# Kernel optimization log

Hardware: AMD Instinct MI355X
Metric: run time of the kernel (lower is better)

## Reference

```python
import jax, jax.numpy as jnp
import numpy as np

T_STEPS, BATCH, DX, DH = 128, 128, 1024, 1024
N_GATES = 5


def setup_inputs() -> dict:
    key = jax.random.key(0)
    ks = jax.random.split(key, 4)
    scale_x = 1.0 / np.sqrt(DX)
    scale_h = 1.0 / np.sqrt(DH)
    inputs = jax.random.normal(ks[0], (T_STEPS, BATCH, DX), dtype=jnp.float32)
    memories = jax.random.normal(ks[1], (T_STEPS, BATCH, DH), dtype=jnp.float32)
    h0 = jnp.zeros((BATCH, DH), dtype=jnp.float32)
    c0 = jnp.zeros((BATCH, DH), dtype=jnp.float32)
    Wx = jax.random.normal(ks[2], (N_GATES * DH, DX), dtype=jnp.float32) * scale_x
    bx = jnp.zeros((N_GATES * DH,), dtype=jnp.float32)
    Wh = jax.random.normal(ks[3], (N_GATES * DH, DH), dtype=jnp.float32) * scale_h
    # forget-gate bias (second chunk) initialized to 1, as in reset_parameters_
    bh = jnp.zeros((N_GATES * DH,), dtype=jnp.float32).at[DH:2 * DH].set(1.0)
    return {"inputs": inputs, "memories": memories, "h0": h0, "c0": c0,
            "Wx": Wx, "bx": bx, "Wh": Wh, "bh": bh}


def reference(inputs, memories, h0, c0, Wx, bx, Wh, bh):
    # EpLSTMCell.loop: time-major scan of the custom gated cell.
    # Gate order: I, F, G, O, R (tied forget gate: it = 1 - ft).
    def step(carry, inp):
        h, c = carry
        xt, mt = inp
        gx = jnp.dot(xt, Wx.T) + bx      # [B, 5*Dh]
        gh = jnp.dot(h, Wh.T) + bh       # [B, 5*Dh]
        Xi, Xf, Xg, Xo, Xr = jnp.split(gx, N_GATES, axis=-1)
        Hi, Hf, Hg, Ho, Hr = jnp.split(gh, N_GATES, axis=-1)
        ft = jax.nn.sigmoid(Xf + Hf)
        ot = jax.nn.sigmoid(Xo + Ho)
        it = 1.0 - ft                    # tied forget gate
        gt = jnp.tanh(Xg + Hg)
        rt = jax.nn.sigmoid(Xr + Hr)     # episodic memory gate
        ct = ft * c + it * gt + rt * jnp.tanh(mt)
        ht = ot * jnp.tanh(ct)
        return (ht, ct), ht

    (_, _), outs = jax.lax.scan(step, (h0, c0), (inputs, memories))
    return outs  # [T, B, Dh]
```

## Files before the change

kernel.cpp:

```cpp
#include <hip/hip_runtime.h>

#define T_STEPS 128
#define BATCH   128
#define DX      1024
#define DH      1024
#define BDH     (BATCH * DH)
#define BDX     (BATCH * DX)
#define PLW     40

typedef __attribute__((ext_vector_type(8)))  short short8;
typedef __attribute__((ext_vector_type(16))) float f32x16;

static __device__ __forceinline__ unsigned short f2bf(float f) {
    union { float f; unsigned u; } v; v.f = f;
    unsigned r = v.u + 0x7fffu + ((v.u >> 16) & 1u);
    return (unsigned short)(r >> 16);
}
static __device__ __forceinline__ float sigf(float x) {
    float u = __expf(-fabsf(x));
    float b = 1.0f / (1.0f + u);
    return x >= 0.0f ? b : 1.0f - b;
}
static __device__ __forceinline__ float tanhfast(float x) {
    float u = __expf(-2.0f * fabsf(x));
    float r = (1.0f - u) / (1.0f + u);
    return x >= 0.0f ? r : -r;
}


__global__ __launch_bounds__(256) void prep_x(const float* __restrict__ x,
                                              unsigned short* __restrict__ Xb) {
    const size_t i8 = ((size_t)blockIdx.x * 256 + threadIdx.x) * 8;
    float4 lo = reinterpret_cast<const float4*>(x + i8)[0];
    float4 hi = reinterpret_cast<const float4*>(x + i8)[1];
    union { unsigned short u[8]; short8 v; } pk;
    pk.u[0]=f2bf(lo.x); pk.u[1]=f2bf(lo.y); pk.u[2]=f2bf(lo.z); pk.u[3]=f2bf(lo.w);
    pk.u[4]=f2bf(hi.x); pk.u[5]=f2bf(hi.y); pk.u[6]=f2bf(hi.z); pk.u[7]=f2bf(hi.w);
    *reinterpret_cast<short8*>(Xb + i8) = pk.v;
}

__global__ __launch_bounds__(256) void init_seed(const float* __restrict__ h0,
                                                 unsigned short* __restrict__ hseq,
                                                 unsigned* __restrict__ gflag) {
    const int i = blockIdx.x * 256 + threadIdx.x;
    if (i < BDH) hseq[i] = f2bf(h0[i]);
    if (blockIdx.x == 0) gflag[threadIdx.x] = 0;
}

__global__ __launch_bounds__(128) void prep_wxp(const float* __restrict__ Wx,
                                                const float* __restrict__ bx,
                                                const float* __restrict__ bh,
                                                unsigned short* __restrict__ Wxp,
                                                float* __restrict__ bp) {
    const int p = blockIdx.x;
    const int js = p >> 5, g = (p >> 3) & 3, jj = p & 7;
    const int srow = (g + 1) * 1024 + js * 8 + jj;
    const int k = threadIdx.x * 8;
    float4 lo = *(const float4*)(Wx + (size_t)srow * DX + k);
    float4 hi = *(const float4*)(Wx + (size_t)srow * DX + k + 4);
    union { unsigned short u[8]; short8 v; } pk;
    pk.u[0]=f2bf(lo.x); pk.u[1]=f2bf(lo.y); pk.u[2]=f2bf(lo.z); pk.u[3]=f2bf(lo.w);
    pk.u[4]=f2bf(hi.x); pk.u[5]=f2bf(hi.y); pk.u[6]=f2bf(hi.z); pk.u[7]=f2bf(hi.w);
    *reinterpret_cast<short8*>(Wxp + (size_t)p * 1024 + k) = pk.v;
    if (threadIdx.x == 0) bp[p] = bx[srow] + bh[srow];
}

template<bool XBF16>
__global__ __launch_bounds__(256, 1) void gx_prepass2(
    const void* __restrict__ xsrc, const unsigned short* __restrict__ Wxp,
    const float* __restrict__ bp, _Float16* __restrict__ Gx)
{
    extern __shared__ char sm[];
    _Float16* pl16 = (_Float16*)(sm + 131072);

    const int bid = blockIdx.x;
    const int c  = bid & 7;
    const int jp = bid >> 3;
    const int tid = threadIdx.x;

    {
        const int row = tid >> 2;
        const int chunk = tid & 3;
        const int sw = (row & 7) << 4;
        const unsigned short* src = Wxp + (size_t)(jp * 64 + row) * 1024;
        char* dst = sm + row * 2048;
        #pragma unroll
        for (int j = 0; j < 32; ++j) {
            const int off = chunk * 16 + j * 64;
            short8 v = *(const short8*)(src + (off >> 1));
            *(short8*)(dst + (off ^ sw)) = v;
        }
    }

    const int rrow = tid >> 1;
    const int jjb  = (tid & 1) * 4;
    float bias_f[2][16];
    #pragma unroll
    for (int jsl = 0; jsl < 2; ++jsl)
        #pragma unroll
        for (int q = 0; q < 4; ++q)
            #pragma unroll
            for (int g = 0; g < 4; ++g)
                bias_f[jsl][q * 4 + g] = bp[(jp * 2 + jsl) * 32 + g * 8 + (jjb + q)];

    const int wave = tid >> 6, lane = tid & 63;
    const int k8 = (lane >> 5) * 8;
    const char* wrow0 = sm + (lane & 31) * 2048;
    const char* wrow1 = wrow0 + 32 * 2048;
    const int sw2 = ((lane & 31) & 7) << 4;
    __syncthreads();

    for (int i = 0; i < 16; ++i) {
        const int mt = c * 16 + i;
        const int arow = mt * 128 + wave * 32 + (lane & 31);
        f32x16 a00 = {}, a01 = {}, a10 = {}, a11 = {};

        if (XBF16) {
            const unsigned short* xp = (const unsigned short*)xsrc + (size_t)arow * 1024 + k8;
            #pragma unroll 8
            for (int ks = 0; ks < 64; ++ks) {
                short8 a  = *(const short8*)(xp + ks * 16);
                short8 b0 = *(const short8*)(wrow0 + ((ks * 32 + k8 * 2) ^ sw2));
                short8 b1 = *(const short8*)(wrow1 + ((ks * 32 + k8 * 2) ^ sw2));
                if (ks & 1) {
                    a01 = __builtin_amdgcn_mfma_f32_32x32x16_bf16(a, b0, a01, 0, 0, 0);
                    a11 = __builtin_amdgcn_mfma_f32_32x32x16_bf16(a, b1, a11, 0, 0, 0);
                } else {
                    a00 = __builtin_amdgcn_mfma_f32_32x32x16_bf16(a, b0, a00, 0, 0, 0);
                    a10 = __builtin_amdgcn_mfma_f32_32x32x16_bf16(a, b1, a10, 0, 0, 0);
                }
            }
        } else {
            const float* Af = (const float*)xsrc + (size_t)arow * 1024 + k8;
            #pragma unroll 8
            for (int ks = 0; ks < 64; ++ks) {
                float4 lo = *(const float4*)(Af + ks * 16);
                float4 hi = *(const float4*)(Af + ks * 16 + 4);
                union { unsigned u32[4]; short8 v; } pk;
                pk.u32[0] = __builtin_amdgcn_perm(__float_as_uint(lo.y), __float_as_uint(lo.x), 0x07060302u);
                pk.u32[1] = __builtin_amdgcn_perm(__float_as_uint(lo.w), __float_as_uint(lo.z), 0x07060302u);
                pk.u32[2] = __builtin_amdgcn_perm(__float_as_uint(hi.y), __float_as_uint(hi.x), 0x07060302u);
                pk.u32[3] = __builtin_amdgcn_perm(__float_as_uint(hi.w), __float_as_uint(hi.z), 0x07060302u);
                short8 b0 = *(const short8*)(wrow0 + ((ks * 32 + k8 * 2) ^ sw2));
                short8 b1 = *(const short8*)(wrow1 + ((ks * 32 + k8 * 2) ^ sw2));
                if (ks & 1) {
                    a01 = __builtin_amdgcn_mfma_f32_32x32x16_bf16(pk.v, b0, a01, 0, 0, 0);
                    a11 = __builtin_amdgcn_mfma_f32_32x32x16_bf16(pk.v, b1, a11, 0, 0, 0);
                } else {
                    a00 = __builtin_amdgcn_mfma_f32_32x32x16_bf16(pk.v, b0, a00, 0, 0, 0);
                    a10 = __builtin_amdgcn_mfma_f32_32x32x16_bf16(pk.v, b1, a10, 0, 0, 0);
                }
            }
        }
        f32x16 r0 = a00 + a01;
        f32x16 r1 = a10 + a11;

        #pragma unroll
        for (int ii = 0; ii < 16; ++ii) {
            const int rowc = (ii & 3) + 8 * (ii >> 2) + 4 * (lane >> 5);
            pl16[(wave * 32 + rowc) * 72 + (lane & 31)]      = (_Float16)r0[ii];
            pl16[(wave * 32 + rowc) * 72 + 32 + (lane & 31)] = (_Float16)r1[ii];
        }
        __syncthreads();

        #pragma unroll
        for (int jsl = 0; jsl < 2; ++jsl) {
            __attribute__((aligned(16))) _Float16 vals[16];
            #pragma unroll
            for (int q = 0; q < 4; ++q)
                #pragma unroll
                for (int g = 0; g < 4; ++g)
                    vals[q * 4 + g] = (_Float16)(
                        (float)pl16[rrow * 72 + jsl * 32 + g * 8 + (jjb + q)]
                        + bias_f[jsl][q * 4 + g]);
            _Float16* dst = Gx + ((size_t)(mt * 128 + rrow) * 4096
                                  + (jp * 2 + jsl) * 32 + jjb * 4);
            *(uint4*)dst       = *(uint4*)&vals[0];
            *(uint4*)(dst + 8) = *(uint4*)&vals[8];
        }
        __syncthreads();
    }
}

__global__ __launch_bounds__(256, 1) void eplstm_h(
    const _Float16* __restrict__ Gx,  const float* __restrict__ mem,
    const float* __restrict__ Wh,     const float* __restrict__ c0,
    unsigned short* __restrict__ hseq, float* __restrict__ out,
    unsigned* __restrict__ gflag)
{
    extern __shared__ char smem[];
    float* pl = (float*)(smem + 65536);

    const int bid = blockIdx.x;
    const int js = bid >> 1, bhh = bid & 1;
    const int tid = threadIdx.x;

    {
        const int row = tid >> 3;
        const int g = row >> 3, jj = row & 7;
        const int srow = (g + 1) * 1024 + js * 8 + jj;
        const int sw = (row & 7) << 4;
        const float* W = Wh + (size_t)srow * 1024;
        char* dst = smem + row * 2048;
        #pragma unroll
        for (int it = 0; it < 16; ++it) {
            const int k = (tid & 7) * 128 + it * 8;
            float4 lo = *(const float4*)(W + k);
            float4 hi = *(const float4*)(W + k + 4);
            union { unsigned short u[8]; short8 v; } pk;
            pk.u[0]=f2bf(lo.x); pk.u[1]=f2bf(lo.y); pk.u[2]=f2bf(lo.z); pk.u[3]=f2bf(lo.w);
            pk.u[4]=f2bf(hi.x); pk.u[5]=f2bf(hi.y); pk.u[6]=f2bf(hi.z); pk.u[7]=f2bf(hi.w);
            *(short8*)(dst + ((k * 2) ^ sw)) = pk.v;
        }
    }

    const int e0 = tid * 2;
    const int row_e = e0 >> 3;
    const int jj0 = e0 & 7;
    const int brow = bhh * 64 + row_e;
    const size_t obase = (size_t)brow * DH + js * 8 + jj0;
    const int mh_e = row_e >> 5, r_e = row_e & 31;
    float2 creg = *(const float2*)(c0 + obase);

    const int wave = tid >> 6, lane = tid & 63;
    const int mh = wave >> 1, kh = wave & 1;
    const int arow = bhh * 64 + mh * 32 + (lane & 31);
    const int k8 = (lane >> 5) * 8;
    const char* wrow = smem + (lane & 31) * 2048;
    const int sw2 = ((lane & 31) & 7) << 4;
    const int kbyte0 = (kh * 512 + k8) * 2;
    const int p = lane & 31;
    const int word = (p & 7) * 4 + (p >> 3);
    float* plw = pl + wave * 32 * PLW;
    unsigned long long* fb = (unsigned long long*)(gflag + bhh * 128);

    __syncthreads();

    for (int t = 0; t < T_STEPS; ++t) {
        uint4 gxv = *(const uint4*)(Gx + ((size_t)(t * BATCH + brow) * 4096 + js * 32 + jj0 * 4));
        float2 mv = *(const float2*)(mem + (size_t)t * BDH + obase);

        if (t > 0) {
            for (;;) {
                unsigned long long fv = __hip_atomic_load(&fb[lane], __ATOMIC_RELAXED,
                                                          __HIP_MEMORY_SCOPE_AGENT);
                if (__all(((unsigned)fv >= (unsigned)t) &&
                          ((unsigned)(fv >> 32) >= (unsigned)t))) break;
                __builtin_amdgcn_s_sleep(1);
            }
        }

        const unsigned short* hp = hseq + (size_t)t * BDH + (size_t)arow * DH + kh * 512 + k8;
        f32x16 a0 = {}, a1 = {};
        #pragma unroll 16
        for (int ks = 0; ks < 32; ++ks) {
            short8 a = *(const short8*)(hp + ks * 16);
            short8 b = *(const short8*)(wrow + ((kbyte0 + ks * 32) ^ sw2));
            if (ks & 1) a1 = __builtin_amdgcn_mfma_f32_32x32x16_bf16(a, b, a1, 0, 0, 0);
            else        a0 = __builtin_amdgcn_mfma_f32_32x32x16_bf16(a, b, a0, 0, 0, 0);
        }
        f32x16 r = a0 + a1;
        #pragma unroll
        for (int ii = 0; ii < 16; ++ii) {
            const int rowc = (ii & 3) + 8 * (ii >> 2) + 4 * (lane >> 5);
            plw[rowc * PLW + word] = r[ii];
        }
        __syncthreads();

        float4 p0A = *(const float4*)(pl + (((mh_e << 1) | 0) * 32 + r_e) * PLW + (jj0 + 0) * 4);
        float4 p0B = *(const float4*)(pl + (((mh_e << 1) | 1) * 32 + r_e) * PLW + (jj0 + 0) * 4);
        float4 p1A = *(const float4*)(pl + (((mh_e << 1) | 0) * 32 + r_e) * PLW + (jj0 + 1) * 4);
        float4 p1B = *(const float4*)(pl + (((mh_e << 1) | 1) * 32 + r_e) * PLW + (jj0 + 1) * 4);
        union { uint4 u; _Float16 h[8]; } G; G.u = gxv;

        float hv[2];
        {
            const float gF = (float)G.h[0] + p0A.x + p0B.x;
            const float gG = (float)G.h[1] + p0A.y + p0B.y;
            const float gO = (float)G.h[2] + p0A.z + p0B.z;
            const float gR = (float)G.h[3] + p0A.w + p0B.w;
            const float ft = sigf(gF), ot = sigf(gO), rt = sigf(gR);
            const float gt = tanhfast(gG);
            const float cv = ft * creg.x + (1.f - ft) * gt + rt * tanhfast(mv.x);
            creg.x = cv;
            hv[0] = ot * tanhfast(cv);
        }
        {
            const float gF = (float)G.h[4] + p1A.x + p1B.x;
            const float gG = (float)G.h[5] + p1A.y + p1B.y;
            const float gO = (float)G.h[6] + p1A.z + p1B.z;
            const float gR = (float)G.h[7] + p1A.w + p1B.w;
            const float ft = sigf(gF), ot = sigf(gO), rt = sigf(gR);
            const float gt = tanhfast(gG);
            const float cv = ft * creg.y + (1.f - ft) * gt + rt * tanhfast(mv.y);
            creg.y = cv;
            hv[1] = ot * tanhfast(cv);
        }
        *(float2*)(out + (size_t)t * BDH + obase) = make_float2(hv[0], hv[1]);
        const unsigned hp2 = (unsigned)f2bf(hv[0]) | ((unsigned)f2bf(hv[1]) << 16);
        __hip_atomic_store((unsigned*)(hseq + (size_t)(t + 1) * BDH + obase), hp2,
                           __ATOMIC_RELAXED, __HIP_MEMORY_SCOPE_AGENT);

        asm volatile("s_waitcnt vmcnt(0)" ::: "memory");
        __syncthreads();
        if (tid == 0 && t < T_STEPS - 1) {
            __hip_atomic_store(&gflag[bhh * 128 + js], (unsigned)(t + 1),
                               __ATOMIC_RELAXED, __HIP_MEMORY_SCOPE_AGENT);
        }
    }
}

template<bool XBF16>
__global__ __launch_bounds__(256, 1) void eplstm_persistent(
    const void*  __restrict__ xsrc, const float* __restrict__ mem,
    const float* __restrict__ Wx,   const float* __restrict__ Wh,
    const float* __restrict__ bxp,  const float* __restrict__ bhp,
    const float* __restrict__ c0,
    unsigned short* __restrict__ hseq, float* __restrict__ out,
    unsigned* __restrict__ bar)
{
    extern __shared__ char smem[];
    float* pl = reinterpret_cast<float*>(smem + 131072);

    const int bid = blockIdx.x;
    const int js  = bid >> 1;
    const int bhh = bid & 1;
    const int tid = threadIdx.x;

    {
        const int prow = tid >> 3;
        const int g = prow >> 3, jj = prow & 7;
        const int srow = (g + 1) * 1024 + js * 8 + jj;
        const int kc = (tid & 7) * 256;
        const int sw = (prow & 7) << 4;
        for (int it = 0; it < 32; ++it) {
            const int k = kc + it * 8;
            const float* src = (k < DX) ? (Wx + (size_t)srow * DX + k)
                                        : (Wh + (size_t)srow * DH + (k - DX));
            float4 lo = reinterpret_cast<const float4*>(src)[0];
            float4 hi = reinterpret_cast<const float4*>(src)[1];
            union { unsigned short u[8]; short8 v; } pk;
            pk.u[0]=f2bf(lo.x); pk.u[1]=f2bf(lo.y); pk.u[2]=f2bf(lo.z); pk.u[3]=f2bf(lo.w);
            pk.u[4]=f2bf(hi.x); pk.u[5]=f2bf(hi.y); pk.u[6]=f2bf(hi.z); pk.u[7]=f2bf(hi.w);
            *reinterpret_cast<short8*>(smem + prow * 4096 + ((k * 2) ^ sw)) = pk.v;
        }
    }

    const int e0   = tid * 2;
    const int bl   = e0 >> 3;
    const int jj0  = e0 & 7;
    const int brow_g = bhh * 64 + bl;
    const size_t oidx = (size_t)brow_g * DH + js * 8 + jj0;
    float biasv[2][4];
    #pragma unroll
    for (int e2 = 0; e2 < 2; ++e2)
        #pragma unroll
        for (int g = 0; g < 4; ++g) {
            const int srow = (g + 1) * 1024 + js * 8 + jj0 + e2;
            biasv[e2][g] = bxp[srow] + bhp[srow];
        }
    float2 creg = *reinterpret_cast<const float2*>(c0 + oidx);
    const int mh_e = bl >> 5, rr = bl & 31;

    const int wave = tid >> 6;
    const int lane = tid & 63;
    const int mh = wave >> 1, kh = wave & 1;
    const int arow   = bhh * 64 + mh * 32 + (lane & 31);
    const int k8     = (lane >> 5) * 8;
    const int brow   = lane & 31;
    const char* bbase = smem + brow * 4096;
    const int swz    = (brow & 7) << 4;
    const int kbyte0 = kh * 2048 + k8 * 2;

    __syncthreads();

    for (int t = 0; t < T_STEPS; ++t) {
        f32x16 ac0 = {}, ac1 = {}, ac2 = {}, ac3 = {};
        if (XBF16 || kh == 1) {
            const unsigned short* Ab = kh
                ? (hseq + (size_t)t * BDH + (size_t)arow * DH + k8)
                : ((const unsigned short*)xsrc + (size_t)t * BDX + (size_t)arow * DX + k8);
            #pragma unroll 8
            for (int ks = 0; ks < 64; ++ks) {
                short8 a = *reinterpret_cast<const short8*>(Ab + ks * 16);
                short8 b = *reinterpret_cast<const short8*>(bbase + ((kbyte0 + ks * 32) ^ swz));
                if      ((ks & 3) == 0) ac0 = __builtin_amdgcn_mfma_f32_32x32x16_bf16(a, b, ac0, 0, 0, 0);
                else if ((ks & 3) == 1) ac1 = __builtin_amdgcn_mfma_f32_32x32x16_bf16(a, b, ac1, 0, 0, 0);
                else if ((ks & 3) == 2) ac2 = __builtin_amdgcn_mfma_f32_32x32x16_bf16(a, b, ac2, 0, 0, 0);
                else                    ac3 = __builtin_amdgcn_mfma_f32_32x32x16_bf16(a, b, ac3, 0, 0, 0);
            }
        } else {
            const float* Af = (const float*)xsrc + (size_t)t * BDX + (size_t)arow * DX + k8;
            #pragma unroll 4
            for (int ks = 0; ks < 64; ++ks) {
                float4 lo = reinterpret_cast<const float4*>(Af + ks * 16)[0];
                float4 hi = reinterpret_cast<const float4*>(Af + ks * 16)[1];
                union { unsigned short u[8]; short8 v; } pk;
                pk.u[0]=f2bf(lo.x); pk.u[1]=f2bf(lo.y); pk.u[2]=f2bf(lo.z); pk.u[3]=f2bf(lo.w);
                pk.u[4]=f2bf(hi.x); pk.u[5]=f2bf(hi.y); pk.u[6]=f2bf(hi.z); pk.u[7]=f2bf(hi.w);
                short8 a = pk.v;
                short8 b = *reinterpret_cast<const short8*>(bbase + ((kbyte0 + ks * 32) ^ swz));
                if      ((ks & 3) == 0) ac0 = __builtin_amdgcn_mfma_f32_32x32x16_bf16(a, b, ac0, 0, 0, 0);
                else if ((ks & 3) == 1) ac1 = __builtin_amdgcn_mfma_f32_32x32x16_bf16(a, b, ac1, 0, 0, 0);
                else if ((ks & 3) == 2) ac2 = __builtin_amdgcn_mfma_f32_32x32x16_bf16(a, b, ac2, 0, 0, 0);
                else                    ac3 = __builtin_amdgcn_mfma_f32_32x32x16_bf16(a, b, ac3, 0, 0, 0);
            }
        }
        f32x16 r = (ac0 + ac1) + (ac2 + ac3);

        #pragma unroll
        for (int i = 0; i < 16; ++i) {
            const int row = (i & 3) + 8 * (i >> 2) + 4 * (lane >> 5);
            pl[(wave * 32 + row) * 33 + brow] = r[i];
        }
        __syncthreads();

        const float2 mt2 = *reinterpret_cast<const float2*>(mem + (size_t)t * BDH + oidx);
        float hv[2];
        #pragma unroll
        for (int e2 = 0; e2 < 2; ++e2) {
            const int jj = jj0 + e2;
            float gs[4];
            #pragma unroll
            for (int g = 0; g < 4; ++g) {
                const int col = g * 8 + jj;
                gs[g] = pl[((mh_e * 2 + 0) * 32 + rr) * 33 + col]
                      + pl[((mh_e * 2 + 1) * 32 + rr) * 33 + col]
                      + biasv[e2][g];
            }
            const float ft = 1.f / (1.f + expf(-gs[0]));
            const float gt = tanhf(gs[1]);
            const float ot = 1.f / (1.f + expf(-gs[2]));
            const float rt = 1.f / (1.f + expf(-gs[3]));
            const float cin = e2 ? creg.y : creg.x;
            const float mv  = e2 ? mt2.y : mt2.x;
            const float cv = ft * cin + (1.f - ft) * gt + rt * tanhf(mv);
            if (e2) creg.y = cv; else creg.x = cv;
            hv[e2] = ot * tanhf(cv);
        }
        *reinterpret_cast<float2*>(out + (size_t)t * BDH + oidx) = make_float2(hv[0], hv[1]);
        const unsigned hp = (unsigned)f2bf(hv[0]) | ((unsigned)f2bf(hv[1]) << 16);
        __hip_atomic_store((unsigned*)(hseq + (size_t)(t + 1) * BDH + oidx), hp,
                           __ATOMIC_RELAXED, __HIP_MEMORY_SCOPE_AGENT);

        __syncthreads();
        if (t < T_STEPS - 1) {
            if (tid == 0) {
                const unsigned want = (unsigned)(t + 1);
                const unsigned arrived = __hip_atomic_fetch_add(
                    &bar[bhh * 32], 1u, __ATOMIC_RELAXED, __HIP_MEMORY_SCOPE_AGENT);
                if (arrived == want * 128u - 1u) {
                    __hip_atomic_store(&bar[64 + bhh * 32], want,
                                       __ATOMIC_RELAXED, __HIP_MEMORY_SCOPE_AGENT);
                } else {
                    while (__hip_atomic_load(&bar[64 + bhh * 32],
                                             __ATOMIC_RELAXED, __HIP_MEMORY_SCOPE_AGENT) < want)
                        __builtin_amdgcn_s_sleep(2);
                }
            }
            __syncthreads();
        }
    }
}

extern "C" void kernel_launch(void* const* d_in, const int* in_sizes, int n_in,
                              void* d_out, int out_size, void* d_ws, size_t ws_size,
                              hipStream_t stream) {
    const float* inputs   = (const float*)d_in[0];
    const float* memories = (const float*)d_in[1];
    const float* h0       = (const float*)d_in[2];
    const float* c0       = (const float*)d_in[3];
    const float* Wx       = (const float*)d_in[4];
    const float* bx       = (const float*)d_in[5];
    const float* Wh       = (const float*)d_in[6];
    const float* bh_      = (const float*)d_in[7];
    float* outp = (float*)d_out;

    char* ws = (char*)d_ws;
    size_t off = 0;
    auto alloc = [&](size_t bytes) {
        char* p = ws + off;
        off = (off + bytes + 255) & ~(size_t)255;
        return p;
    };
    unsigned*       gflag = (unsigned*)alloc(256 * sizeof(unsigned));
    unsigned short* hseq  = (unsigned short*)alloc((size_t)(T_STEPS + 1) * BDH * 2);

    const size_t wxp_b  = (size_t)4096 * 1024 * 2;
    const size_t bp_b   = 4096 * 4;
    const size_t gx_b   = (size_t)16384 * 4096 * 2;
    const size_t xb_b   = (size_t)T_STEPS * BDX * 2;
    const size_t need_base = off + wxp_b + 256 + bp_b + 256 + gx_b + 256;
    const size_t need_xb   = need_base + xb_b + 256;

    if (ws_size >= need_base) {
        unsigned short* Wxp = (unsigned short*)alloc(wxp_b);
        float*          bp  = (float*)alloc(bp_b);
        _Float16*       Gx  = (_Float16*)alloc(gx_b);
        const bool use_xb = (ws_size >= need_xb);
        unsigned short* Xb = use_xb ? (unsigned short*)alloc(xb_b) : nullptr;

        init_seed<<<512, 256, 0, stream>>>(h0, hseq, gflag);
        prep_wxp<<<4096, 128, 0, stream>>>(Wx, bx, bh_, Wxp, bp);

        const unsigned pre_smem = 131072 + 128 * 72 * 2;
        if (use_xb) {
            prep_x<<<8192, 256, 0, stream>>>(inputs, Xb);
            (void)hipFuncSetAttribute((const void*)gx_prepass2<true>,
                                      hipFuncAttributeMaxDynamicSharedMemorySize, pre_smem);
            gx_prepass2<true><<<512, 256, pre_smem, stream>>>((const void*)Xb, Wxp, bp, Gx);
        } else {
            (void)hipFuncSetAttribute((const void*)gx_prepass2<false>,
                                      hipFuncAttributeMaxDynamicSharedMemorySize, pre_smem);
            gx_prepass2<false><<<512, 256, pre_smem, stream>>>((const void*)inputs, Wxp, bp, Gx);
        }

        const unsigned smem_bytes = 65536 + 4 * 32 * PLW * 4;
        (void)hipFuncSetAttribute((const void*)eplstm_h,
                                  hipFuncAttributeMaxDynamicSharedMemorySize, smem_bytes);
        void* kargs[] = { (void*)&Gx, (void*)&memories, (void*)&Wh, (void*)&c0,
                          (void*)&hseq, (void*)&outp, (void*)&gflag };
        hipError_t err = hipLaunchCooperativeKernel((const void*)eplstm_h, dim3(256),
                                                    dim3(256), kargs, smem_bytes, stream);
        if (err != hipSuccess) {
            eplstm_h<<<256, 256, smem_bytes, stream>>>(Gx, memories, Wh, c0,
                                                       hseq, outp, gflag);
        }
    } else {
        const bool use_xb = (ws_size >= off + xb_b + 256);
        unsigned short* Xb = use_xb ? (unsigned short*)alloc(xb_b) : nullptr;

        init_seed<<<512, 256, 0, stream>>>(h0, hseq, gflag);
        if (use_xb) prep_x<<<8192, 256, 0, stream>>>(inputs, Xb);

        const unsigned smem_bytes = 131072 + 9216 + 9216 + 64;
        const void* xsrc = use_xb ? (const void*)Xb : (const void*)inputs;
        if (use_xb) {
            (void)hipFuncSetAttribute((const void*)eplstm_persistent<true>,
                                      hipFuncAttributeMaxDynamicSharedMemorySize, smem_bytes);
            void* kargs[] = { (void*)&xsrc, (void*)&memories, (void*)&Wx, (void*)&Wh,
                              (void*)&bx, (void*)&bh_, (void*)&c0, (void*)&hseq,
                              (void*)&outp, (void*)&gflag };
            hipError_t err = hipLaunchCooperativeKernel(
                (const void*)eplstm_persistent<true>, dim3(256), dim3(256),
                kargs, smem_bytes, stream);
            if (err != hipSuccess) {
                eplstm_persistent<true><<<256, 256, smem_bytes, stream>>>(
                    xsrc, memories, Wx, Wh, bx, bh_, c0, hseq, outp, gflag);
            }
        } else {
            (void)hipFuncSetAttribute((const void*)eplstm_persistent<false>,
                                      hipFuncAttributeMaxDynamicSharedMemorySize, smem_bytes);
            void* kargs[] = { (void*)&xsrc, (void*)&memories, (void*)&Wx, (void*)&Wh,
                              (void*)&bx, (void*)&bh_, (void*)&c0, (void*)&hseq,
                              (void*)&outp, (void*)&gflag };
            hipError_t err = hipLaunchCooperativeKernel(
                (const void*)eplstm_persistent<false>, dim3(256), dim3(256),
                kargs, smem_bytes, stream);
            if (err != hipSuccess) {
                eplstm_persistent<false><<<256, 256, smem_bytes, stream>>>(
                    xsrc, memories, Wx, Wh, bx, bh_, c0, hseq, outp, gflag);
            }
        }
    }
}
```

Measured before the change: 1.554 ms.

## Use nontemporal loads/stores and single-wave flag polling in recurrent kernel

Replaces many streaming global loads and stores (weight conversion, Gx writes/reads, memory and output tensors) with nontemporal variants so they bypass or deprioritise the cache. In the recurrent loop, only wave 0 now polls the cross-block step flags, with a longer sleep, and the other waves wait at a block barrier. The output store moves after the hseq publish. The flag buffer is also doubled and zero-initialised. The intent is to cut cache pollution and polling traffic, at the cost of an extra barrier per step and possibly slower wake-up.

```diff
diff --git a/kernel.cpp b/kernel.cpp
--- a/kernel.cpp
+++ b/kernel.cpp
@@ -10,12 +10,21 @@
 
 typedef __attribute__((ext_vector_type(8)))  short short8;
 typedef __attribute__((ext_vector_type(16))) float f32x16;
+typedef __attribute__((ext_vector_type(4)))  float f32x4v;
+typedef __attribute__((ext_vector_type(2)))  float f32x2;
+typedef __attribute__((ext_vector_type(4)))  unsigned u32x4;
 
 static __device__ __forceinline__ unsigned short f2bf(float f) {
     union { float f; unsigned u; } v; v.f = f;
     unsigned r = v.u + 0x7fffu + ((v.u >> 16) & 1u);
     return (unsigned short)(r >> 16);
 }
+static __device__ __forceinline__ short8 pack_bf16x8(f32x4v lo, f32x4v hi) {
+    union { unsigned short u[8]; short8 v; } pk;
+    pk.u[0]=f2bf(lo[0]); pk.u[1]=f2bf(lo[1]); pk.u[2]=f2bf(lo[2]); pk.u[3]=f2bf(lo[3]);
+    pk.u[4]=f2bf(hi[0]); pk.u[5]=f2bf(hi[1]); pk.u[6]=f2bf(hi[2]); pk.u[7]=f2bf(hi[3]);
+    return pk.v;
+}
 static __device__ __forceinline__ float sigf(float x) {
     float u = __expf(-fabsf(x));
     float b = 1.0f / (1.0f + u);
@@ -31,12 +40,10 @@
 __global__ __launch_bounds__(256) void prep_x(const float* __restrict__ x,
                                               unsigned short* __restrict__ Xb) {
     const size_t i8 = ((size_t)blockIdx.x * 256 + threadIdx.x) * 8;
-    float4 lo = reinterpret_cast<const float4*>(x + i8)[0];
-    float4 hi = reinterpret_cast<const float4*>(x + i8)[1];
-    union { unsigned short u[8]; short8 v; } pk;
-    pk.u[0]=f2bf(lo.x); pk.u[1]=f2bf(lo.y); pk.u[2]=f2bf(lo.z); pk.u[3]=f2bf(lo.w);
-    pk.u[4]=f2bf(hi.x); pk.u[5]=f2bf(hi.y); pk.u[6]=f2bf(hi.z); pk.u[7]=f2bf(hi.w);
-    *reinterpret_cast<short8*>(Xb + i8) = pk.v;
+    f32x4v lo = __builtin_nontemporal_load((const f32x4v*)(x + i8));
+    f32x4v hi = __builtin_nontemporal_load((const f32x4v*)(x + i8 + 4));
+    short8 v = pack_bf16x8(lo, hi);
+    __builtin_nontemporal_store(v, (short8*)(Xb + i8));
 }
 
 __global__ __launch_bounds__(256) void init_seed(const float* __restrict__ h0,
@@ -44,7 +51,7 @@
                                                  unsigned* __restrict__ gflag) {
     const int i = blockIdx.x * 256 + threadIdx.x;
     if (i < BDH) hseq[i] = f2bf(h0[i]);
-    if (blockIdx.x == 0) gflag[threadIdx.x] = 0;
+    if (blockIdx.x < 2) gflag[blockIdx.x * 256 + threadIdx.x] = 0;
 }
 
 __global__ __launch_bounds__(128) void prep_wxp(const float* __restrict__ Wx,
@@ -56,12 +63,10 @@
     const int js = p >> 5, g = (p >> 3) & 3, jj = p & 7;
     const int srow = (g + 1) * 1024 + js * 8 + jj;
     const int k = threadIdx.x * 8;
-    float4 lo = *(const float4*)(Wx + (size_t)srow * DX + k);
-    float4 hi = *(const float4*)(Wx + (size_t)srow * DX + k + 4);
-    union { unsigned short u[8]; short8 v; } pk;
-    pk.u[0]=f2bf(lo.x); pk.u[1]=f2bf(lo.y); pk.u[2]=f2bf(lo.z); pk.u[3]=f2bf(lo.w);
-    pk.u[4]=f2bf(hi.x); pk.u[5]=f2bf(hi.y); pk.u[6]=f2bf(hi.z); pk.u[7]=f2bf(hi.w);
-    *reinterpret_cast<short8*>(Wxp + (size_t)p * 1024 + k) = pk.v;
+    f32x4v lo = __builtin_nontemporal_load((const f32x4v*)(Wx + (size_t)srow * DX + k));
+    f32x4v hi = __builtin_nontemporal_load((const f32x4v*)(Wx + (size_t)srow * DX + k + 4));
+    short8 v = pack_bf16x8(lo, hi);
+    __builtin_nontemporal_store(v, (short8*)(Wxp + (size_t)p * 1024 + k));
     if (threadIdx.x == 0) bp[p] = bx[srow] + bh[srow];
 }
 
@@ -87,7 +92,7 @@
         #pragma unroll
         for (int j = 0; j < 32; ++j) {
             const int off = chunk * 16 + j * 64;
-            short8 v = *(const short8*)(src + (off >> 1));
+            short8 v = __builtin_nontemporal_load((const short8*)(src + (off >> 1)));
             *(short8*)(dst + (off ^ sw)) = v;
         }
     }
@@ -134,13 +139,13 @@
             const float* Af = (const float*)xsrc + (size_t)arow * 1024 + k8;
             #pragma unroll 8
             for (int ks = 0; ks < 64; ++ks) {
-                float4 lo = *(const float4*)(Af + ks * 16);
-                float4 hi = *(const float4*)(Af + ks * 16 + 4);
+                f32x4v lo = *(const f32x4v*)(Af + ks * 16);
+                f32x4v hi = *(const f32x4v*)(Af + ks * 16 + 4);
                 union { unsigned u32[4]; short8 v; } pk;
-                pk.u32[0] = __builtin_amdgcn_perm(__float_as_uint(lo.y), __float_as_uint(lo.x), 0x07060302u);
-                pk.u32[1] = __builtin_amdgcn_perm(__float_as_uint(lo.w), __float_as_uint(lo.z), 0x07060302u);
-                pk.u32[2] = __builtin_amdgcn_perm(__float_as_uint(hi.y), __float_as_uint(hi.x), 0x07060302u);
-                pk.u32[3] = __builtin_amdgcn_perm(__float_as_uint(hi.w), __float_as_uint(hi.z), 0x07060302u);
+                pk.u32[0] = __builtin_amdgcn_perm(__float_as_uint(lo[1]), __float_as_uint(lo[0]), 0x07060302u);
+                pk.u32[1] = __builtin_amdgcn_perm(__float_as_uint(lo[3]), __float_as_uint(lo[2]), 0x07060302u);
+                pk.u32[2] = __builtin_amdgcn_perm(__float_as_uint(hi[1]), __float_as_uint(hi[0]), 0x07060302u);
+                pk.u32[3] = __builtin_amdgcn_perm(__float_as_uint(hi[3]), __float_as_uint(hi[2]), 0x07060302u);
                 short8 b0 = *(const short8*)(wrow0 + ((ks * 32 + k8 * 2) ^ sw2));
                 short8 b1 = *(const short8*)(wrow1 + ((ks * 32 + k8 * 2) ^ sw2));
                 if (ks & 1) {
@@ -165,18 +170,18 @@
 
         #pragma unroll
         for (int jsl = 0; jsl < 2; ++jsl) {
-            __attribute__((aligned(16))) _Float16 vals[16];
+            union { _Float16 h[16]; u32x4 q[2]; } V;
             #pragma unroll
             for (int q = 0; q < 4; ++q)
                 #pragma unroll
                 for (int g = 0; g < 4; ++g)
-                    vals[q * 4 + g] = (_Float16)(
+                    V.h[q * 4 + g] = (_Float16)(
                         (float)pl16[rrow * 72 + jsl * 32 + g * 8 + (jjb + q)]
                         + bias_f[jsl][q * 4 + g]);
             _Float16* dst = Gx + ((size_t)(mt * 128 + rrow) * 4096
                                   + (jp * 2 + jsl) * 32 + jjb * 4);
-            *(uint4*)dst       = *(uint4*)&vals[0];
-            *(uint4*)(dst + 8) = *(uint4*)&vals[8];
+            __builtin_nontemporal_store(V.q[0], (u32x4*)dst);
+            __builtin_nontemporal_store(V.q[1], (u32x4*)(dst + 8));
         }
         __syncthreads();
     }
@@ -205,12 +210,10 @@
         #pragma unroll
         for (int it = 0; it < 16; ++it) {
             const int k = (tid & 7) * 128 + it * 8;
-            float4 lo = *(const float4*)(W + k);
-            float4 hi = *(const float4*)(W + k + 4);
-            union { unsigned short u[8]; short8 v; } pk;
-            pk.u[0]=f2bf(lo.x); pk.u[1]=f2bf(lo.y); pk.u[2]=f2bf(lo.z); pk.u[3]=f2bf(lo.w);
-            pk.u[4]=f2bf(hi.x); pk.u[5]=f2bf(hi.y); pk.u[6]=f2bf(hi.z); pk.u[7]=f2bf(hi.w);
-            *(short8*)(dst + ((k * 2) ^ sw)) = pk.v;
+            f32x4v lo = __builtin_nontemporal_load((const f32x4v*)(W + k));
+            f32x4v hi = __builtin_nontemporal_load((const f32x4v*)(W + k + 4));
+            short8 v = pack_bf16x8(lo, hi);
+            *(short8*)(dst + ((k * 2) ^ sw)) = v;
         }
     }
 
@@ -237,17 +240,22 @@
     __syncthreads();
 
     for (int t = 0; t < T_STEPS; ++t) {
-        uint4 gxv = *(const uint4*)(Gx + ((size_t)(t * BATCH + brow) * 4096 + js * 32 + jj0 * 4));
-        float2 mv = *(const float2*)(mem + (size_t)t * BDH + obase);
+        u32x4 gxv = __builtin_nontemporal_load(
+            (const u32x4*)(Gx + ((size_t)(t * BATCH + brow) * 4096 + js * 32 + jj0 * 4)));
+        f32x2 mv = __builtin_nontemporal_load(
+            (const f32x2*)(mem + (size_t)t * BDH + obase));
 
         if (t > 0) {
-            for (;;) {
-                unsigned long long fv = __hip_atomic_load(&fb[lane], __ATOMIC_RELAXED,
-                                                          __HIP_MEMORY_SCOPE_AGENT);
-                if (__all(((unsigned)fv >= (unsigned)t) &&
-                          ((unsigned)(fv >> 32) >= (unsigned)t))) break;
-                __builtin_amdgcn_s_sleep(1);
-            }
+            if (wave == 0) {
+                for (;;) {
+                    unsigned long long fv = __hip_atomic_load(
+                        &fb[lane], __ATOMIC_RELAXED, __HIP_MEMORY_SCOPE_AGENT);
+                    if (__all(((unsigned)fv >= (unsigned)t) &&
+                              ((unsigned)(fv >> 32) >= (unsigned)t))) break;
+                    __builtin_amdgcn_s_sleep(4);
+                }
+            }
+            __syncthreads();
         }
 
         const unsigned short* hp = hseq + (size_t)t * BDH + (size_t)arow * DH + kh * 512 + k8;
@@ -271,7 +279,7 @@
         float4 p0B = *(const float4*)(pl + (((mh_e << 1) | 1) * 32 + r_e) * PLW + (jj0 + 0) * 4);
         float4 p1A = *(const float4*)(pl + (((mh_e << 1) | 0) * 32 + r_e) * PLW + (jj0 + 1) * 4);
         float4 p1B = *(const float4*)(pl + (((mh_e << 1) | 1) * 32 + r_e) * PLW + (jj0 + 1) * 4);
-        union { uint4 u; _Float16 h[8]; } G; G.u = gxv;
+        union { u32x4 u; _Float16 h[8]; } G; G.u = gxv;
 
         float hv[2];
         {
@@ -281,7 +289,7 @@
             const float gR = (float)G.h[3] + p0A.w + p0B.w;
             const float ft = sigf(gF), ot = sigf(gO), rt = sigf(gR);
             const float gt = tanhfast(gG);
-            const float cv = ft * creg.x + (1.f - ft) * gt + rt * tanhfast(mv.x);
+            const float cv = ft * creg.x + (1.f - ft) * gt + rt * tanhfast(mv[0]);
             creg.x = cv;
             hv[0] = ot * tanhfast(cv);
         }
@@ -292,14 +300,15 @@
             const float gR = (float)G.h[7] + p1A.w + p1B.w;
             const float ft = sigf(gF), ot = sigf(gO), rt = sigf(gR);
             const float gt = tanhfast(gG);
-            const float cv = ft * creg.y + (1.f - ft) * gt + rt * tanhfast(mv.y);
+            const float cv = ft * creg.y + (1.f - ft) * gt + rt * tanhfast(mv[1]);
             creg.y = cv;
             hv[1] = ot * tanhfast(cv);
         }
-        *(float2*)(out + (size_t)t * BDH + obase) = make_float2(hv[0], hv[1]);
         const unsigned hp2 = (unsigned)f2bf(hv[0]) | ((unsigned)f2bf(hv[1]) << 16);
         __hip_atomic_store((unsigned*)(hseq + (size_t)(t + 1) * BDH + obase), hp2,
                            __ATOMIC_RELAXED, __HIP_MEMORY_SCOPE_AGENT);
+        f32x2 hvv = { hv[0], hv[1] };
+        __builtin_nontemporal_store(hvv, (f32x2*)(out + (size_t)t * BDH + obase));
 
         asm volatile("s_waitcnt vmcnt(0)" ::: "memory");
         __syncthreads();
@@ -337,12 +346,10 @@
             const int k = kc + it * 8;
             const float* src = (k < DX) ? (Wx + (size_t)srow * DX + k)
                                         : (Wh + (size_t)srow * DH + (k - DX));
-            float4 lo = reinterpret_cast<const float4*>(src)[0];
-            float4 hi = reinterpret_cast<const float4*>(src)[1];
-            union { unsigned short u[8]; short8 v; } pk;
-            pk.u[0]=f2bf(lo.x); pk.u[1]=f2bf(lo.y); pk.u[2]=f2bf(lo.z); pk.u[3]=f2bf(lo.w);
-            pk.u[4]=f2bf(hi.x); pk.u[5]=f2bf(hi.y); pk.u[6]=f2bf(hi.z); pk.u[7]=f2bf(hi.w);
-            *reinterpret_cast<short8*>(smem + prow * 4096 + ((k * 2) ^ sw)) = pk.v;
+            f32x4v lo = *(const f32x4v*)(src);
+            f32x4v hi = *(const f32x4v*)(src + 4);
+            short8 v = pack_bf16x8(lo, hi);
+            *reinterpret_cast<short8*>(smem + prow * 4096 + ((k * 2) ^ sw)) = v;
         }
     }
 
@@ -393,12 +400,9 @@
             const float* Af = (const float*)xsrc + (size_t)t * BDX + (size_t)arow * DX + k8;
             #pragma unroll 4
             for (int ks = 0; ks < 64; ++ks) {
-                float4 lo = reinterpret_cast<const float4*>(Af + ks * 16)[0];
-                float4 hi = reinterpret_cast<const float4*>(Af + ks * 16)[1];
-                union { unsigned short u[8]; short8 v; } pk;
-                pk.u[0]=f2bf(lo.x); pk.u[1]=f2bf(lo.y); pk.u[2]=f2bf(lo.z); pk.u[3]=f2bf(lo.w);
-                pk.u[4]=f2bf(hi.x); pk.u[5]=f2bf(hi.y); pk.u[6]=f2bf(hi.z); pk.u[7]=f2bf(hi.w);
-                short8 a = pk.v;
+                f32x4v lo = *(const f32x4v*)(Af + ks * 16);
+                f32x4v hi = *(const f32x4v*)(Af + ks * 16 + 4);
+                short8 a = pack_bf16x8(lo, hi);
                 short8 b = *reinterpret_cast<const short8*>(bbase + ((kbyte0 + ks * 32) ^ swz));
                 if      ((ks & 3) == 0) ac0 = __builtin_amdgcn_mfma_f32_32x32x16_bf16(a, b, ac0, 0, 0, 0);
                 else if ((ks & 3) == 1) ac1 = __builtin_amdgcn_mfma_f32_32x32x16_bf16(a, b, ac1, 0, 0, 0);
@@ -483,7 +487,7 @@
         off = (off + bytes + 255) & ~(size_t)255;
         return p;
     };
-    unsigned*       gflag = (unsigned*)alloc(256 * sizeof(unsigned));
+    unsigned*       gflag = (unsigned*)alloc(512 * sizeof(unsigned));
     unsigned short* hseq  = (unsigned short*)alloc((size_t)(T_STEPS + 1) * BDH * 2);
 
     const size_t wxp_b  = (size_t)4096 * 1024 * 2;
```

New measurement: 1.563 ms. About the same (+0.5%).
